# Kernel optimization log

Measured on AMD Instinct MI355X. Metric: run time of the kernel, lower is better.

Reference implementation:

```python
import jax, jax.numpy as jnp
import numpy as np

N = 50000   # nodes
E = 800000  # edges (avg degree 16)
G = 256     # graphs in batch
H = 16      # hidden_channels
ADD = 7     # ADD_FEATURES
EPS = 1e-5


def setup_inputs() -> dict:
    key = jax.random.key(0)
    ks = jax.random.split(key, 32)
    inp = {
        "x": jax.random.normal(ks[0], (N, 1), dtype=jnp.float32),
        "edge_index": jax.random.randint(ks[1], (2, E), 0, N),
        "batch": jnp.sort(jax.random.randint(ks[2], (N,), 0, G)),
        "y_extra": jax.random.normal(ks[3], (G, ADD), dtype=jnp.float32),
    }
    k = 4
    conv_dims = [(1, H), (H, 2 * H), (2 * H, 4 * H), (4 * H, 8 * H)]
    for i, (ci, co) in enumerate(conv_dims, 1):
        inp[f"W{i}"] = (jax.random.normal(ks[k], (ci, co), dtype=jnp.float32) / np.float32(np.sqrt(ci))); k += 1
        inp[f"b{i}"] = jnp.zeros((co,), dtype=jnp.float32)
    for i, c in enumerate([H, 2 * H, 4 * H], 1):
        inp[f"g{i}"] = jnp.ones((c,), jnp.float32) + 0.1 * jax.random.normal(ks[k], (c,), dtype=jnp.float32); k += 1
        inp[f"be{i}"] = 0.1 * jax.random.normal(ks[k], (c,), dtype=jnp.float32); k += 1
    mlp_dims = [(8 * H + ADD, 128), (128, 64), (64, 32), (32, 2)]
    for i, (ci, co) in enumerate(mlp_dims, 1):
        inp[f"lw{i}"] = (jax.random.normal(ks[k], (ci, co), dtype=jnp.float32) / np.float32(np.sqrt(ci))); k += 1
        inp[f"lb{i}"] = 0.01 * jax.random.normal(ks[k], (co,), dtype=jnp.float32); k += 1
    return inp


def _gcn_norm(edge_index, n):
    # PyG GCNConv default: add self loops, symmetric deg^{-1/2} normalization.
    loops = jnp.arange(n)
    src = jnp.concatenate([edge_index[0], loops])
    dst = jnp.concatenate([edge_index[1], loops])
    deg = jax.ops.segment_sum(jnp.ones_like(src, dtype=jnp.float32), dst, num_segments=n)
    dis = jnp.where(deg > 0, jax.lax.rsqrt(jnp.maximum(deg, 1.0)), 0.0)
    return src, dst, dis[src] * dis[dst]


def _gcn_conv(x, W, b, src, dst, norm, n):
    h = x @ W                                   # [N, Cout]
    msg = h[src] * norm[:, None]                # [E+N, Cout] gather
    agg = jax.ops.segment_sum(msg, dst, num_segments=n)  # scatter-add
    return agg + b


def _bn(x, gamma, beta):
    # training-mode BatchNorm1d over node dim (biased variance)
    mu = jnp.mean(x, axis=0)
    var = jnp.mean(jnp.square(x - mu), axis=0)
    return gamma * (x - mu) * jax.lax.rsqrt(var + EPS) + beta


def _gelu(x):
    return jax.nn.gelu(x, approximate=False)  # torch F.gelu default = exact erf


def reference(x, edge_index, batch, y_extra,
              W1, b1, W2, b2, W3, b3, W4, b4,
              g1, be1, g2, be2, g3, be3,
              lw1, lb1, lw2, lb2, lw3, lb3, lw4, lb4):
    n = x.shape[0]
    src, dst, norm = _gcn_norm(edge_index, n)
    h = _gelu(_gcn_conv(x, W1, b1, src, dst, norm, n))
    h = _bn(h, g1, be1)
    h = _gelu(_gcn_conv(h, W2, b2, src, dst, norm, n))
    h = _bn(h, g2, be2)
    h = _gelu(_gcn_conv(h, W3, b3, src, dst, norm, n))
    h = _bn(h, g3, be3)
    h = _gelu(_gcn_conv(h, W4, b4, src, dst, norm, n))
    # global mean pool per graph
    sums = jax.ops.segment_sum(h, batch, num_segments=G)
    cnt = jax.ops.segment_sum(jnp.ones((n,), jnp.float32), batch, num_segments=G)
    pooled = sums / jnp.maximum(cnt, 1.0)[:, None]   # [G, 8H]
    z = jnp.concatenate([pooled, y_extra], axis=1)   # [G, 8H+7]
    z = _gelu(z @ lw1 + lb1)
    z = _gelu(z @ lw2 + lb2)
    z = _gelu(z @ lw3 + lb3)
    return jax.nn.sigmoid(z @ lw4 + lb4)             # [G, 2]
```

## Files before the change

kernel.cpp:

```cpp
#include <hip/hip_runtime.h>
#include <math.h>

#define NN 50000
#define EE 800000
#define GG 256
#define NPB 100
#define NBUCK 500
#define EPB 4096
#define NEB 196
#define NB_NODE 196

__device__ __forceinline__ float gelu_f(float v){
    return 0.5f * v * (1.0f + erff(v * 0.70710678118654752f));
}

__global__ __launch_bounds__(256) void k_hist(const int* __restrict__ dst, int* __restrict__ bucket_cnt_p, int e){
    __shared__ int hist[512];
    int t = threadIdx.x;
    int start = blockIdx.x * EPB;
    for (int k = t; k < 512; k += 256) hist[k] = 0;
    __syncthreads();
#pragma unroll
    for (int k = 0; k < EPB / 256; k++){
        int idx = start + k * 256 + t;
        if (idx < e) atomicAdd(&hist[dst[idx] / NPB], 1);
    }
    __syncthreads();
    for (int k = t; k < NBUCK; k += 256){
        int h = hist[k];
        if (h) atomicAdd(&bucket_cnt_p[k * 16], h);
    }
}

__global__ __launch_bounds__(512) void k_bscan(const int* __restrict__ bucket_cnt_p,
                                               int* __restrict__ bucket_off, int* __restrict__ cursor_p){
    __shared__ int s[512];
    int t = threadIdx.x;
    int v = (t < NBUCK) ? bucket_cnt_p[t * 16] : 0;
    s[t] = v;
    __syncthreads();
    for (int off = 1; off < 512; off <<= 1){
        int u = (t >= off) ? s[t - off] : 0;
        __syncthreads();
        s[t] += u;
        __syncthreads();
    }
    if (t < NBUCK){
        int ex = s[t] - v;
        bucket_off[t] = ex;
        cursor_p[t * 16] = ex;
    }
}

__global__ __launch_bounds__(256) void k_scatter(const int* __restrict__ src, const int* __restrict__ dst,
                                                 int* __restrict__ cursor_p, int2* __restrict__ ebuf, int e){
    __shared__ int hist[512], base[512];
    int t = threadIdx.x;
    int start = blockIdx.x * EPB;
    for (int k = t; k < 512; k += 256) hist[k] = 0;
    __syncthreads();
    int ss[EPB / 256], dd[EPB / 256], bb[EPB / 256];
    int cntl = 0;
#pragma unroll
    for (int k = 0; k < EPB / 256; k++){
        int idx = start + k * 256 + t;
        if (idx < e){
            int s_ = src[idx], d_ = dst[idx];
            int b_ = d_ / NPB;
            ss[cntl] = s_; dd[cntl] = d_; bb[cntl] = b_;
            atomicAdd(&hist[b_], 1);
            cntl++;
        }
    }
    __syncthreads();
    for (int k = t; k < NBUCK; k += 256){
        int h = hist[k];
        base[k] = h ? atomicAdd(&cursor_p[k * 16], h) : 0;
    }
    __syncthreads();
    for (int k = t; k < 512; k += 256) hist[k] = 0;
    __syncthreads();
    for (int k = 0; k < cntl; k++){
        int b_ = bb[k];
        int pos = base[b_] + atomicAdd(&hist[b_], 1);
        ebuf[pos] = make_int2(ss[k], dd[k]);
    }
}

__global__ __launch_bounds__(256) void k_build(const int2* __restrict__ ebuf,
                                               const int* __restrict__ bucket_cnt_p,
                                               const int* __restrict__ bucket_off,
                                               int* __restrict__ rp, int* __restrict__ col,
                                               float* __restrict__ dis, float* __restrict__ invdis,
                                               const float* __restrict__ x, float* __restrict__ xs, int n){
    int b = blockIdx.x;
    int t = threadIdx.x;
    int nbase = b * NPB;
    int eoff = bucket_off[b];
    int ecnt = bucket_cnt_p[b * 16];
    __shared__ int cnt[128], excl[128], cnt2[128], s[128];
    if (t < 128){ cnt[t] = 0; cnt2[t] = 0; }
    __syncthreads();
    for (int j = t; j < ecnt; j += 256)
        atomicAdd(&cnt[ebuf[eoff + j].y - nbase], 1);
    __syncthreads();
    int v = (t < 128) ? cnt[t] : 0;
    if (t < 128) s[t] = v;
    __syncthreads();
    for (int off = 1; off < 128; off <<= 1){
        int u = (t < 128 && t >= off) ? s[t - off] : 0;
        __syncthreads();
        if (t < 128) s[t] += u;
        __syncthreads();
    }
    if (t < 128) excl[t] = s[t] - v;
    __syncthreads();
    if (t < NPB){
        int node = nbase + t;
        int dgg = cnt[t];
        rp[node] = eoff + excl[t];
        float dv = rsqrtf((float)(dgg + 1));
        dis[node] = dv;
        invdis[node] = sqrtf((float)(dgg + 1));
        xs[node] = dv * x[node];
    }
    if (b == NBUCK - 1 && t == 0) rp[n] = eoff + ecnt;
    __syncthreads();
    for (int j = t; j < ecnt; j += 256){
        int2 e2 = ebuf[eoff + j];
        int li = e2.y - nbase;
        int p = eoff + excl[li] + atomicAdd(&cnt2[li], 1);
        col[p] = e2.x;
    }
}

__global__ __launch_bounds__(256) void k_g1l1(const float* __restrict__ xs, const float* __restrict__ dis,
                                              const int* __restrict__ rp, const int* __restrict__ col,
                                              const float* __restrict__ W, const float* __restrict__ bias,
                                              float* __restrict__ dsum, float* __restrict__ hs, int n){
    int node = blockIdx.x * 256 + threadIdx.x;
    if (node >= n) return;
    int beg = rp[node], end = rp[node + 1];
    float a0 = 0.f, a1 = 0.f, d0 = 0.f, d1 = 0.f;
    int j = beg;
    for (; j + 1 < end; j += 2){
        int c0 = col[j], c1 = col[j + 1];
        a0 += xs[c0]; d0 += dis[c0];
        a1 += xs[c1]; d1 += dis[c1];
    }
    if (j < end){ int c = col[j]; a0 += xs[c]; d0 += dis[c]; }
    float dn = dis[node];
    dsum[node] = d0 + d1 + dn;
    float a = dn * (a0 + a1 + xs[node]);
    float4* o = (float4*)(hs + (size_t)node * 16);
#pragma unroll
    for (int u = 0; u < 4; u++){
        float4 r;
        r.x = gelu_f(bias[u*4+0] + a * W[u*4+0]) * dn;
        r.y = gelu_f(bias[u*4+1] + a * W[u*4+1]) * dn;
        r.z = gelu_f(bias[u*4+2] + a * W[u*4+2]) * dn;
        r.w = gelu_f(bias[u*4+3] + a * W[u*4+3]) * dn;
        o[u] = r;
    }
}

template<int C>
__global__ __launch_bounds__(256) void k_gather(const float* __restrict__ hs, const int* __restrict__ rp,
                                                const int* __restrict__ col, const float* __restrict__ dis,
                                                const float* __restrict__ dsum, const float* __restrict__ stat,
                                                const float* __restrict__ gamma, const float* __restrict__ beta,
                                                float* __restrict__ outp, int n){
    constexpr int TPN = C / 4;
    int i = blockIdx.x * 256 + threadIdx.x;
    int node = i / TPN, q = i % TPN;
    if (node >= n) return;
    int c0 = q * 4;
    const float invn = 1.0f / (float)NN;
    float scv[4], shv[4];
#pragma unroll
    for (int u = 0; u < 4; u++){
        float mean = stat[c0 + u] * invn;
        float var  = stat[128 + c0 + u] * invn - mean * mean;
        float sc   = gamma[c0 + u] * rsqrtf(var + 1e-5f);
        scv[u] = sc;
        shv[u] = beta[c0 + u] - mean * sc;
    }
    const float4* h4 = (const float4*)hs;
    int beg = rp[node], end = rp[node + 1];
    float a0 = 0.f, a1 = 0.f, a2 = 0.f, a3 = 0.f;
    float b0 = 0.f, b1 = 0.f, b2 = 0.f, b3 = 0.f;
    int j = beg;
    for (; j + 7 < end; j += 8){
        int i0 = col[j],   i1 = col[j+1], i2 = col[j+2], i3 = col[j+3];
        int i4 = col[j+4], i5 = col[j+5], i6 = col[j+6], i7 = col[j+7];
        float4 v0 = h4[i0 * TPN + q];
        float4 v1 = h4[i1 * TPN + q];
        float4 v2 = h4[i2 * TPN + q];
        float4 v3 = h4[i3 * TPN + q];
        float4 v4 = h4[i4 * TPN + q];
        float4 v5 = h4[i5 * TPN + q];
        float4 v6 = h4[i6 * TPN + q];
        float4 v7 = h4[i7 * TPN + q];
        a0 += v0.x; a1 += v0.y; a2 += v0.z; a3 += v0.w;
        b0 += v1.x; b1 += v1.y; b2 += v1.z; b3 += v1.w;
        a0 += v2.x; a1 += v2.y; a2 += v2.z; a3 += v2.w;
        b0 += v3.x; b1 += v3.y; b2 += v3.z; b3 += v3.w;
        a0 += v4.x; a1 += v4.y; a2 += v4.z; a3 += v4.w;
        b0 += v5.x; b1 += v5.y; b2 += v5.z; b3 += v5.w;
        a0 += v6.x; a1 += v6.y; a2 += v6.z; a3 += v6.w;
        b0 += v7.x; b1 += v7.y; b2 += v7.z; b3 += v7.w;
    }
    for (; j < end; j++){
        float4 v = h4[col[j] * TPN + q];
        a0 += v.x; a1 += v.y; a2 += v.z; a3 += v.w;
    }
    float4 vs = h4[node * TPN + q];
    a0 += vs.x; a1 += vs.y; a2 += vs.z; a3 += vs.w;
    a0 += b0; a1 += b1; a2 += b2; a3 += b3;
    float dn = dis[node];
    float dsm = dsum[node];
    float4 r = make_float4((a0 * scv[0] + shv[0] * dsm) * dn,
                           (a1 * scv[1] + shv[1] * dsm) * dn,
                           (a2 * scv[2] + shv[2] * dsm) * dn,
                           (a3 * scv[3] + shv[3] * dsm) * dn);
    ((float4*)outp)[node * TPN + q] = r;
}

template<int CIN, int COUT, bool SCALE>
__global__ __launch_bounds__(256) void k_linT(const float* __restrict__ xin, const float* __restrict__ dis,
                                              const float* __restrict__ W,
                                              const float* __restrict__ bias, float* __restrict__ outp, int n){
    constexpr int QC = COUT / 4;
    constexpr int K4 = CIN / 4;
    int i = blockIdx.x * 256 + threadIdx.x;
    int tile = i / QC, q = i % QC;
    int n0 = tile * 4;
    if (n0 >= n) return;
    const float4* xp0 = (const float4*)(xin + (size_t)(n0 + 0) * CIN);
    const float4* xp1 = (const float4*)(xin + (size_t)(n0 + 1) * CIN);
    const float4* xp2 = (const float4*)(xin + (size_t)(n0 + 2) * CIN);
    const float4* xp3 = (const float4*)(xin + (size_t)(n0 + 3) * CIN);
    const float4* Wq = (const float4*)W + q;
    float4 bb = ((const float4*)bias)[q];
    float acc[4][4];
#pragma unroll
    for (int nd = 0; nd < 4; nd++){
        acc[nd][0] = bb.x; acc[nd][1] = bb.y; acc[nd][2] = bb.z; acc[nd][3] = bb.w;
    }
#pragma unroll 1
    for (int k4 = 0; k4 < K4; k4++){
        float4 xv[4];
        xv[0] = xp0[k4]; xv[1] = xp1[k4]; xv[2] = xp2[k4]; xv[3] = xp3[k4];
        float4 w0 = Wq[(k4 * 4 + 0) * QC];
        float4 w1 = Wq[(k4 * 4 + 1) * QC];
        float4 w2 = Wq[(k4 * 4 + 2) * QC];
        float4 w3 = Wq[(k4 * 4 + 3) * QC];
#pragma unroll
        for (int nd = 0; nd < 4; nd++){
            acc[nd][0] += xv[nd].x*w0.x + xv[nd].y*w1.x + xv[nd].z*w2.x + xv[nd].w*w3.x;
            acc[nd][1] += xv[nd].x*w0.y + xv[nd].y*w1.y + xv[nd].z*w2.y + xv[nd].w*w3.y;
            acc[nd][2] += xv[nd].x*w0.z + xv[nd].y*w1.z + xv[nd].z*w2.z + xv[nd].w*w3.z;
            acc[nd][3] += xv[nd].x*w0.w + xv[nd].y*w1.w + xv[nd].z*w2.w + xv[nd].w*w3.w;
        }
    }
    float4* o4 = (float4*)outp;
#pragma unroll
    for (int nd = 0; nd < 4; nd++){
        float sc = SCALE ? dis[n0 + nd] : 1.0f;
        o4[(size_t)(n0 + nd) * QC + q] =
            make_float4(gelu_f(acc[nd][0])*sc, gelu_f(acc[nd][1])*sc,
                        gelu_f(acc[nd][2])*sc, gelu_f(acc[nd][3])*sc);
    }
}

template<int C>
__global__ __launch_bounds__(256) void k_stats(const float* __restrict__ hs, const float* __restrict__ invdis,
                                               float* __restrict__ stat, int n){
    constexpr int REP = 256 / C;
    int t = threadIdx.x;
    int rep = t / C;
    int c = t % C;
    float s = 0.f, q = 0.f;
    for (int row = blockIdx.x * REP + rep; row < n; row += gridDim.x * REP){
        float v = hs[(long long)row * C + c] * invdis[row];
        s += v; q += v * v;
    }
    __shared__ float ss[256], sq[256];
    ss[t] = s; sq[t] = q;
    __syncthreads();
    for (int off = 128; off >= C; off >>= 1){
        if (t < off){ ss[t] += ss[t + off]; sq[t] += sq[t + off]; }
        __syncthreads();
    }
    if (t < C){
        atomicAdd(&stat[t], ss[t]);
        atomicAdd(&stat[128 + t], sq[t]);
    }
}

__global__ __launch_bounds__(128) void k_pool(const float* __restrict__ h4, const int* __restrict__ batch,
                                              float* __restrict__ pool, int n){
    int g = blockIdx.x;
    int t = threadIdx.x;
    int lo = 0, hi = n;
    while (lo < hi){ int mid = (lo + hi) >> 1; if (batch[mid] < g) lo = mid + 1; else hi = mid; }
    int s = lo;
    hi = n;
    while (lo < hi){ int mid = (lo + hi) >> 1; if (batch[mid] < g + 1) lo = mid + 1; else hi = mid; }
    int e = lo;
    float a0 = 0.f, a1 = 0.f, a2 = 0.f, a3 = 0.f;
    int node = s;
    for (; node + 3 < e; node += 4){
        a0 += h4[(size_t)(node + 0) * 128 + t];
        a1 += h4[(size_t)(node + 1) * 128 + t];
        a2 += h4[(size_t)(node + 2) * 128 + t];
        a3 += h4[(size_t)(node + 3) * 128 + t];
    }
    for (; node < e; node++) a0 += h4[(size_t)node * 128 + t];
    float sum = (a0 + a1) + (a2 + a3);
    pool[g * 128 + t] = sum / fmaxf((float)(e - s), 1.0f);
}

__global__ __launch_bounds__(128) void k_mlp(const float* __restrict__ pool,
                                             const float* __restrict__ yex,
                                             const float* __restrict__ lw1, const float* __restrict__ lb1,
                                             const float* __restrict__ lw2, const float* __restrict__ lb2,
                                             const float* __restrict__ lw3, const float* __restrict__ lb3,
                                             const float* __restrict__ lw4, const float* __restrict__ lb4,
                                             float* __restrict__ outp){
    int g = blockIdx.x;
    int t = threadIdx.x;
    __shared__ float z[136];
    __shared__ float z2[128];
    __shared__ float z3[64];
    __shared__ float z4[32];
    z[t] = pool[g * 128 + t];
    if (t < 7) z[128 + t] = yex[g * 7 + t];
    __syncthreads();
    {
        float acc = lb1[t];
        for (int k = 0; k < 135; k++) acc += z[k] * lw1[k * 128 + t];
        z2[t] = gelu_f(acc);
    }
    __syncthreads();
    if (t < 64){
        float acc = lb2[t];
        for (int k = 0; k < 128; k++) acc += z2[k] * lw2[k * 64 + t];
        z3[t] = gelu_f(acc);
    }
    __syncthreads();
    if (t < 32){
        float acc = lb3[t];
        for (int k = 0; k < 64; k++) acc += z3[k] * lw3[k * 32 + t];
        z4[t] = gelu_f(acc);
    }
    __syncthreads();
    if (t < 2){
        float acc = lb4[t];
        for (int k = 0; k < 32; k++) acc += z4[k] * lw4[k * 2 + t];
        outp[g * 2 + t] = 1.0f / (1.0f + expf(-acc));
    }
}

extern "C" void kernel_launch(void* const* d_in, const int* in_sizes, int n_in,
                              void* d_out, int out_size, void* d_ws, size_t ws_size,
                              hipStream_t stream) {
    const float* x     = (const float*)d_in[0];
    const int*   ei    = (const int*)  d_in[1];
    const int*   batch = (const int*)  d_in[2];
    const float* yex   = (const float*)d_in[3];
    const float* W1 = (const float*)d_in[4];  const float* b1 = (const float*)d_in[5];
    const float* W2 = (const float*)d_in[6];  const float* b2 = (const float*)d_in[7];
    const float* W3 = (const float*)d_in[8];  const float* b3 = (const float*)d_in[9];
    const float* W4 = (const float*)d_in[10]; const float* b4 = (const float*)d_in[11];
    const float* g1 = (const float*)d_in[12]; const float* be1 = (const float*)d_in[13];
    const float* g2 = (const float*)d_in[14]; const float* be2 = (const float*)d_in[15];
    const float* g3 = (const float*)d_in[16]; const float* be3 = (const float*)d_in[17];
    const float* lw1 = (const float*)d_in[18]; const float* lb1 = (const float*)d_in[19];
    const float* lw2 = (const float*)d_in[20]; const float* lb2 = (const float*)d_in[21];
    const float* lw3 = (const float*)d_in[22]; const float* lb3 = (const float*)d_in[23];
    const float* lw4 = (const float*)d_in[24]; const float* lb4 = (const float*)d_in[25];
    float* out = (float*)d_out;

    char* wsb = (char*)d_ws;
    size_t off = 0;
    auto alloc = [&](size_t elems) -> void* {
        void* p = wsb + off;
        off += ((elems * 4 + 255) / 256) * 256;
        return p;
    };
    float* stats        = (float*)alloc(3 * 256);
    int*   bucket_cnt_p = (int*)  alloc(NBUCK * 16);
    size_t zero_bytes = off;
    int*   bucket_off   = (int*)  alloc(NBUCK);
    int*   cursor_p     = (int*)  alloc(NBUCK * 16);
    int2*  ebuf         = (int2*) alloc((size_t)EE * 2);
    float* pool   = (float*)alloc(GG * 128);
    int*   rp     = (int*)  alloc(NN + 1);
    float* dis    = (float*)alloc(NN);
    float* invdis = (float*)alloc(NN);
    float* dsum   = (float*)alloc(NN);
    float* xs     = (float*)alloc(NN);
    int*   col    = (int*)  alloc(EE);
    float* hbuf   = (float*)alloc((size_t)NN * 128);
    float* abuf   = (float*)alloc((size_t)NN * 64);

    hipMemsetAsync(d_ws, 0, zero_bytes, stream);

    auto nb = [](long long total){ return (int)((total + 255) / 256); };

    k_hist   <<<NEB, 256, 0, stream>>>(ei + EE, bucket_cnt_p, EE);
    k_bscan  <<<1, 512, 0, stream>>>(bucket_cnt_p, bucket_off, cursor_p);
    k_scatter<<<NEB, 256, 0, stream>>>(ei, ei + EE, cursor_p, ebuf, EE);
    k_build  <<<NBUCK, 256, 0, stream>>>(ebuf, bucket_cnt_p, bucket_off, rp, col, dis, invdis, x, xs, NN);

    k_g1l1<<<NB_NODE, 256, 0, stream>>>(xs, dis, rp, col, W1, b1, dsum, hbuf, NN);
    k_stats<16><<<128, 256, 0, stream>>>(hbuf, invdis, stats + 0, NN);

    k_gather<16><<<nb((long long)NN * 4), 256, 0, stream>>>(hbuf, rp, col, dis, dsum, stats + 0, g1, be1, abuf, NN);
    k_linT<16, 32, true><<<nb((long long)(NN / 4) * 8), 256, 0, stream>>>(abuf, dis, W2, b2, hbuf, NN);
    k_stats<32><<<128, 256, 0, stream>>>(hbuf, invdis, stats + 256, NN);

    k_gather<32><<<nb((long long)NN * 8), 256, 0, stream>>>(hbuf, rp, col, dis, dsum, stats + 256, g2, be2, abuf, NN);
    k_linT<32, 64, true><<<nb((long long)(NN / 4) * 16), 256, 0, stream>>>(abuf, dis, W3, b3, hbuf, NN);
    k_stats<64><<<128, 256, 0, stream>>>(hbuf, invdis, stats + 512, NN);

    k_gather<64><<<nb((long long)NN * 16), 256, 0, stream>>>(hbuf, rp, col, dis, dsum, stats + 512, g3, be3, abuf, NN);
    k_linT<64, 128, false><<<nb((long long)(NN / 4) * 32), 256, 0, stream>>>(abuf, dis, W4, b4, hbuf, NN);
    k_pool<<<GG, 128, 0, stream>>>(hbuf, batch, pool, NN);

    k_mlp<<<GG, 128, 0, stream>>>(pool, yex,
                                  lw1, lb1, lw2, lb2, lw3, lb3, lw4, lb4, out);
}
```

Baseline: 366.8 us.

## Fuse final linear layer into mean pooling and pack edge/node buffers

Replaces the last transform kernel plus pooling with one per-graph kernel that computes GELU(x·W4+b) on the fly and averages it, so the N×128 intermediate is never written or re-read. Edge records in the bucketed CSR build are packed into one int (src<<7 | local dst), halving ebuf traffic. Node scaled-x and deg^-1/2 are interleaved into a float2 so the first-layer gather does one load per neighbor. Risk: the fused pool kernel uses only 256 blocks with 64 weight registers per thread and serial per-graph loops, which may underutilize the GPU compared to the wide linear kernel.

New measurement: 432.7 us. +18.0%, slower.

```diff
diff --git a/kernel.cpp b/kernel.cpp
--- a/kernel.cpp
+++ b/kernel.cpp
@@ -53,13 +53,13 @@
 }
 
 __global__ __launch_bounds__(256) void k_scatter(const int* __restrict__ src, const int* __restrict__ dst,
-                                                 int* __restrict__ cursor_p, int2* __restrict__ ebuf, int e){
+                                                 int* __restrict__ cursor_p, int* __restrict__ ebuf, int e){
     __shared__ int hist[512], base[512];
     int t = threadIdx.x;
     int start = blockIdx.x * EPB;
     for (int k = t; k < 512; k += 256) hist[k] = 0;
     __syncthreads();
-    int ss[EPB / 256], dd[EPB / 256], bb[EPB / 256];
+    int pk[EPB / 256], bb[EPB / 256];
     int cntl = 0;
 #pragma unroll
     for (int k = 0; k < EPB / 256; k++){
@@ -67,7 +67,8 @@
         if (idx < e){
             int s_ = src[idx], d_ = dst[idx];
             int b_ = d_ / NPB;
-            ss[cntl] = s_; dd[cntl] = d_; bb[cntl] = b_;
+            pk[cntl] = (s_ << 7) | (d_ - b_ * NPB);
+            bb[cntl] = b_;
             atomicAdd(&hist[b_], 1);
             cntl++;
         }
@@ -83,16 +84,17 @@
     for (int k = 0; k < cntl; k++){
         int b_ = bb[k];
         int pos = base[b_] + atomicAdd(&hist[b_], 1);
-        ebuf[pos] = make_int2(ss[k], dd[k]);
-    }
-}
-
-__global__ __launch_bounds__(256) void k_build(const int2* __restrict__ ebuf,
+        ebuf[pos] = pk[k];
+    }
+}
+
+__global__ __launch_bounds__(256) void k_build(const int* __restrict__ ebuf,
                                                const int* __restrict__ bucket_cnt_p,
                                                const int* __restrict__ bucket_off,
                                                int* __restrict__ rp, int* __restrict__ col,
                                                float* __restrict__ dis, float* __restrict__ invdis,
-                                               const float* __restrict__ x, float* __restrict__ xs, int n){
+                                               float2* __restrict__ xd,
+                                               const float* __restrict__ x, int n){
     int b = blockIdx.x;
     int t = threadIdx.x;
     int nbase = b * NPB;
@@ -102,7 +104,7 @@
     if (t < 128){ cnt[t] = 0; cnt2[t] = 0; }
     __syncthreads();
     for (int j = t; j < ecnt; j += 256)
-        atomicAdd(&cnt[ebuf[eoff + j].y - nbase], 1);
+        atomicAdd(&cnt[ebuf[eoff + j] & 127], 1);
     __syncthreads();
     int v = (t < 128) ? cnt[t] : 0;
     if (t < 128) s[t] = v;
@@ -122,19 +124,19 @@
         float dv = rsqrtf((float)(dgg + 1));
         dis[node] = dv;
         invdis[node] = sqrtf((float)(dgg + 1));
-        xs[node] = dv * x[node];
+        xd[node] = make_float2(dv * x[node], dv);
     }
     if (b == NBUCK - 1 && t == 0) rp[n] = eoff + ecnt;
     __syncthreads();
     for (int j = t; j < ecnt; j += 256){
-        int2 e2 = ebuf[eoff + j];
-        int li = e2.y - nbase;
+        int v2 = ebuf[eoff + j];
+        int li = v2 & 127;
         int p = eoff + excl[li] + atomicAdd(&cnt2[li], 1);
-        col[p] = e2.x;
-    }
-}
-
-__global__ __launch_bounds__(256) void k_g1l1(const float* __restrict__ xs, const float* __restrict__ dis,
+        col[p] = v2 >> 7;
+    }
+}
+
+__global__ __launch_bounds__(256) void k_g1l1(const float2* __restrict__ xd,
                                               const int* __restrict__ rp, const int* __restrict__ col,
                                               const float* __restrict__ W, const float* __restrict__ bias,
                                               float* __restrict__ dsum, float* __restrict__ hs, int n){
@@ -144,14 +146,16 @@
     float a0 = 0.f, a1 = 0.f, d0 = 0.f, d1 = 0.f;
     int j = beg;
     for (; j + 1 < end; j += 2){
-        int c0 = col[j], c1 = col[j + 1];
-        a0 += xs[c0]; d0 += dis[c0];
-        a1 += xs[c1]; d1 += dis[c1];
-    }
-    if (j < end){ int c = col[j]; a0 += xs[c]; d0 += dis[c]; }
-    float dn = dis[node];
+        float2 v0 = xd[col[j]];
+        float2 v1 = xd[col[j + 1]];
+        a0 += v0.x; d0 += v0.y;
+        a1 += v1.x; d1 += v1.y;
+    }
+    if (j < end){ float2 v0 = xd[col[j]]; a0 += v0.x; d0 += v0.y; }
+    float2 self = xd[node];
+    float dn = self.y;
     dsum[node] = d0 + d1 + dn;
-    float a = dn * (a0 + a1 + xs[node]);
+    float a = dn * (a0 + a1 + self.x);
     float4* o = (float4*)(hs + (size_t)node * 16);
 #pragma unroll
     for (int u = 0; u < 4; u++){
@@ -273,6 +277,43 @@
     }
 }
 
+__global__ __launch_bounds__(256) void k_l4p(const float* __restrict__ abuf, const float* __restrict__ W,
+                                             const float* __restrict__ bias, const int* __restrict__ batch,
+                                             float* __restrict__ pool, int n){
+    int g = blockIdx.x;
+    int t = threadIdx.x;
+    int half = t >> 7;
+    int c = t & 127;
+    int lo = 0, hi = n;
+    while (lo < hi){ int m = (lo + hi) >> 1; if (batch[m] < g) lo = m + 1; else hi = m; }
+    int s = lo;
+    hi = n;
+    while (lo < hi){ int m = (lo + hi) >> 1; if (batch[m] < g + 1) lo = m + 1; else hi = m; }
+    int e = lo;
+    float wcol[64];
+#pragma unroll
+    for (int k = 0; k < 64; k++) wcol[k] = W[k * 128 + c];
+    float b = bias[c];
+    float acc = 0.f;
+    for (int node = s + half; node < e; node += 2){
+        const float4* row = (const float4*)(abuf + (size_t)node * 64);
+        float dot = b;
+#pragma unroll
+        for (int k4 = 0; k4 < 16; k4++){
+            float4 xv = row[k4];
+            dot += xv.x*wcol[k4*4+0] + xv.y*wcol[k4*4+1] + xv.z*wcol[k4*4+2] + xv.w*wcol[k4*4+3];
+        }
+        acc += gelu_f(dot);
+    }
+    __shared__ float red[256];
+    red[t] = acc;
+    __syncthreads();
+    if (t < 128){
+        float sum = red[t] + red[t + 128];
+        pool[g * 128 + t] = sum / fmaxf((float)(e - s), 1.0f);
+    }
+}
+
 template<int C>
 __global__ __launch_bounds__(256) void k_stats(const float* __restrict__ hs, const float* __restrict__ invdis,
                                                float* __restrict__ stat, int n){
@@ -296,29 +337,6 @@
         atomicAdd(&stat[t], ss[t]);
         atomicAdd(&stat[128 + t], sq[t]);
     }
-}
-
-__global__ __launch_bounds__(128) void k_pool(const float* __restrict__ h4, const int* __restrict__ batch,
-                                              float* __restrict__ pool, int n){
-    int g = blockIdx.x;
-    int t = threadIdx.x;
-    int lo = 0, hi = n;
-    while (lo < hi){ int mid = (lo + hi) >> 1; if (batch[mid] < g) lo = mid + 1; else hi = mid; }
-    int s = lo;
-    hi = n;
-    while (lo < hi){ int mid = (lo + hi) >> 1; if (batch[mid] < g + 1) lo = mid + 1; else hi = mid; }
-    int e = lo;
-    float a0 = 0.f, a1 = 0.f, a2 = 0.f, a3 = 0.f;
-    int node = s;
-    for (; node + 3 < e; node += 4){
-        a0 += h4[(size_t)(node + 0) * 128 + t];
-        a1 += h4[(size_t)(node + 1) * 128 + t];
-        a2 += h4[(size_t)(node + 2) * 128 + t];
-        a3 += h4[(size_t)(node + 3) * 128 + t];
-    }
-    for (; node < e; node++) a0 += h4[(size_t)node * 128 + t];
-    float sum = (a0 + a1) + (a2 + a3);
-    pool[g * 128 + t] = sum / fmaxf((float)(e - s), 1.0f);
 }
 
 __global__ __launch_bounds__(128) void k_mlp(const float* __restrict__ pool,
@@ -394,15 +412,15 @@
     size_t zero_bytes = off;
     int*   bucket_off   = (int*)  alloc(NBUCK);
     int*   cursor_p     = (int*)  alloc(NBUCK * 16);
-    int2*  ebuf         = (int2*) alloc((size_t)EE * 2);
+    int*   ebuf         = (int*)  alloc(EE);
     float* pool   = (float*)alloc(GG * 128);
     int*   rp     = (int*)  alloc(NN + 1);
     float* dis    = (float*)alloc(NN);
     float* invdis = (float*)alloc(NN);
     float* dsum   = (float*)alloc(NN);
-    float* xs     = (float*)alloc(NN);
+    float2* xd    = (float2*)alloc(NN * 2);
     int*   col    = (int*)  alloc(EE);
-    float* hbuf   = (float*)alloc((size_t)NN * 128);
+    float* hbuf   = (float*)alloc((size_t)NN * 64);
     float* abuf   = (float*)alloc((size_t)NN * 64);
 
     hipMemsetAsync(d_ws, 0, zero_bytes, stream);
@@ -412,9 +430,9 @@
     k_hist   <<<NEB, 256, 0, stream>>>(ei + EE, bucket_cnt_p, EE);
     k_bscan  <<<1, 512, 0, stream>>>(bucket_cnt_p, bucket_off, cursor_p);
     k_scatter<<<NEB, 256, 0, stream>>>(ei, ei + EE, cursor_p, ebuf, EE);
-    k_build  <<<NBUCK, 256, 0, stream>>>(ebuf, bucket_cnt_p, bucket_off, rp, col, dis, invdis, x, xs, NN);
-
-    k_g1l1<<<NB_NODE, 256, 0, stream>>>(xs, dis, rp, col, W1, b1, dsum, hbuf, NN);
+    k_build  <<<NBUCK, 256, 0, stream>>>(ebuf, bucket_cnt_p, bucket_off, rp, col, dis, invdis, xd, x, NN);
+
+    k_g1l1<<<NB_NODE, 256, 0, stream>>>(xd, rp, col, W1, b1, dsum, hbuf, NN);
     k_stats<16><<<128, 256, 0, stream>>>(hbuf, invdis, stats + 0, NN);
 
     k_gather<16><<<nb((long long)NN * 4), 256, 0, stream>>>(hbuf, rp, col, dis, dsum, stats + 0, g1, be1, abuf, NN);
@@ -426,8 +444,7 @@
     k_stats<64><<<128, 256, 0, stream>>>(hbuf, invdis, stats + 512, NN);
 
     k_gather<64><<<nb((long long)NN * 16), 256, 0, stream>>>(hbuf, rp, col, dis, dsum, stats + 512, g3, be3, abuf, NN);
-    k_linT<64, 128, false><<<nb((long long)(NN / 4) * 32), 256, 0, stream>>>(abuf, dis, W4, b4, hbuf, NN);
-    k_pool<<<GG, 128, 0, stream>>>(hbuf, batch, pool, NN);
+    k_l4p<<<GG, 256, 0, stream>>>(abuf, W4, b4, batch, pool, NN);
 
     k_mlp<<<GG, 128, 0, stream>>>(pool, yex,
                                   lw1, lb1, lw2, lb2, lw3, lb3, lw4, lb4, out);
```
